# Kernel optimization log

Hardware: AMD Instinct MI355X
Metric: run time of the kernel (lower is better)

The kernel has to match this reference:

```python
import jax, jax.numpy as jnp
import numpy as np

N, V, E = 65536, 2048, 1024
TEMPERATURE = 0.5
EPS = 1e-10
LOG_PARAM_Q = -2.995732273553991


def _l2_normalize(x, axis):
    # matches torch F.normalize(p=2): x / max(||x||, 1e-12)
    n = jnp.sqrt(jnp.sum(x * x, axis=axis, keepdims=True))
    return x / jnp.maximum(n, 1e-12)


def setup_inputs() -> dict:
    key = jax.random.key(0)
    k1, k2, k3 = jax.random.split(key, 3)
    z = jax.random.normal(k1, (N, E), dtype=jnp.float32)
    emb_weight = jax.random.normal(k2, (V, E), dtype=jnp.float32)
    U = jax.random.uniform(k3, (N, V), dtype=jnp.float32)
    return {"z": z, "emb_weight": emb_weight, "U": U}


def reference(z, emb_weight, U):
    kappa_q = jnp.exp(jnp.float32(LOG_PARAM_Q)) + jnp.float32(1.0)
    zn = _l2_normalize(z, axis=1)              # [N, E]
    emb = _l2_normalize(emb_weight, axis=1)    # [V, E]
    # logit = -distances = kappa_q * z @ emb.T
    logit = kappa_q * jnp.matmul(zn, emb.T)    # [N, V]
    # gumbel-softmax sample (training branch)
    g = -jnp.log(-jnp.log(U + EPS) + EPS)
    tokens = jax.nn.softmax((logit + g) / TEMPERATURE, axis=-1)  # [N, V]
    z_q = jnp.matmul(tokens, emb)              # [N, E]
    return (tokens, z_q)
```

## Files before the change

### kernel.cpp

```cpp
#include <hip/hip_runtime.h>
#include <hip/hip_bf16.h>
#include <stdint.h>

typedef short bf16x8 __attribute__((ext_vector_type(8)));
typedef float floatx4 __attribute__((ext_vector_type(4)));

#define N_ROWS 65536
#define V_DIM 2048
#define E_DIM 1024

__device__ __forceinline__ short f2bf(float x) {
  union { float f; uint32_t u; } c; c.f = x;
  uint32_t r = (c.u + 0x7FFFu + ((c.u >> 16) & 1u)) >> 16;
  return (short)(uint16_t)r;
}
__device__ __forceinline__ float bf16f(short b) {
  union { uint32_t u; float f; } c; c.u = ((uint32_t)(uint16_t)b) << 16;
  return c.f;
}

__device__ __forceinline__ float wave_sum(float v) {
#pragma unroll
  for (int o = 32; o > 0; o >>= 1) v += __shfl_xor(v, o);
  return v;
}
__device__ __forceinline__ float wave_max(float v) {
#pragma unroll
  for (int o = 32; o > 0; o >>= 1) v = fmaxf(v, __shfl_xor(v, o));
  return v;
}

__device__ __forceinline__ void gll16(const short* g, short* l) {
  __builtin_amdgcn_global_load_lds(
      (const __attribute__((address_space(1))) void*)g,
      (__attribute__((address_space(3))) void*)l, 16, 0, 0);
}

__global__ __launch_bounds__(256) void k_norm_emb(const float* __restrict__ W,
                                                  short* __restrict__ embn,
                                                  short* __restrict__ embnT) {
  const int v = blockIdx.x;
  const int t = threadIdx.x;
  const int w = t >> 6, l = t & 63;
  const float4 val = *(const float4*)&W[(size_t)v * E_DIM + t * 4];
  float ss = val.x * val.x + val.y * val.y + val.z * val.z + val.w * val.w;
  ss = wave_sum(ss);
  __shared__ float red[4];
  if (l == 0) red[w] = ss;
  __syncthreads();
  ss = red[0] + red[1] + red[2] + red[3];
  const float inv = 1.0f / fmaxf(sqrtf(ss), 1e-12f);
  short4 o;
  o.x = f2bf(val.x * inv);
  o.y = f2bf(val.y * inv);
  o.z = f2bf(val.z * inv);
  o.w = f2bf(val.w * inv);
  *(short4*)&embn[(size_t)v * E_DIM + t * 4] = o;
  embnT[(size_t)(t * 4 + 0) * V_DIM + v] = o.x;
  embnT[(size_t)(t * 4 + 1) * V_DIM + v] = o.y;
  embnT[(size_t)(t * 4 + 2) * V_DIM + v] = o.z;
  embnT[(size_t)(t * 4 + 3) * V_DIM + v] = o.w;
}

__global__ __launch_bounds__(256) void k_norm_z(const float* __restrict__ Z,
                                                short* __restrict__ zn) {
  const int w = threadIdx.x >> 6, l = threadIdx.x & 63;
  const int row = blockIdx.x * 4 + w;
  const float* zr = Z + (size_t)row * E_DIM;
  float4 v[4];
  float ss = 0.f;
#pragma unroll
  for (int i = 0; i < 4; ++i) {
    v[i] = *(const float4*)&zr[(i * 64 + l) * 4];
    ss += v[i].x * v[i].x + v[i].y * v[i].y + v[i].z * v[i].z + v[i].w * v[i].w;
  }
  ss = wave_sum(ss);
  const float SCALE = 2.0f * (expf(-2.995732273553991f) + 1.0f);
  const float inv = SCALE / fmaxf(sqrtf(ss), 1e-12f);
  short* zo = zn + (size_t)row * E_DIM;
#pragma unroll
  for (int i = 0; i < 4; ++i) {
    short4 o;
    o.x = f2bf(v[i].x * inv);
    o.y = f2bf(v[i].y * inv);
    o.z = f2bf(v[i].z * inv);
    o.w = f2bf(v[i].w * inv);
    *(short4*)&zo[(i * 64 + l) * 4] = o;
  }
}

template <int KDIM, int NBX, int EPI>
__global__ __launch_bounds__(512, 2) void k_gemm8(
    const short* __restrict__ A, const short* __restrict__ B,
    const float* __restrict__ U, short* __restrict__ Pb,
    float* __restrict__ partials, const float* __restrict__ invsum,
    float* __restrict__ C, float* __restrict__ tokens, int cpx) {
  __shared__ __align__(16) short Sm[65536];
  const int NT = KDIM / 32;
  const int tid = threadIdx.x;
  const int wv = tid >> 6, lane = tid & 63;
  const int lr = lane & 15, lh = lane >> 4;
  const int wr = wv >> 2, wc = wv & 3;
  const int d = blockIdx.x;
  const int L = (d & 7) * cpx + (d >> 3);
  const int by = L / NBX, bx = L % NBX;
  const int m0 = by * 256, n0 = bx * 256;
  const int sg = (((lane & 3) ^ ((lane >> 2) & 3) ^ ((lane >> 4) & 3)) << 3);
  const int srow = wv * 16 + (lane >> 2);
  const short* gA = A + (size_t)(m0 + srow) * KDIM + sg;
  const short* gB = B + (size_t)(n0 + srow) * KDIM + sg;
  const int fslot = lh ^ ((lr ^ (lr >> 2)) & 3);
  const int aoff = wr * 8192 + lr * 64 + fslot * 16;
  const int boff = wc * 4096 + lr * 64 + fslot * 16;

  float inv0 = 0.f, inv1 = 0.f;
  if (EPI == 1) {
    inv0 = invsum[m0 + srow];
    inv1 = invsum[m0 + 128 + srow];
  }

#pragma unroll
  for (int t = 0; t < 2; ++t) {
#pragma unroll
    for (int q = 0; q < 2; ++q) {
      gll16(gA + (size_t)(q * 128) * KDIM + t * 32, Sm + t * 8192 + q * 4096 + wv * 512);
      gll16(gB + (size_t)(q * 128) * KDIM + t * 32, Sm + 32768 + t * 8192 + q * 4096 + wv * 512);
    }
  }
  asm volatile("s_waitcnt vmcnt(4)" ::: "memory");
  __builtin_amdgcn_s_barrier();
  __builtin_amdgcn_sched_barrier(0);

  floatx4 acc[8][4] = {};

#define DO_TILE(KT, STAGE, VMN, TOKW_)                                              \
  {                                                                                 \
    const int cb_ = (KT) & 3;                                                       \
    const char* Ab_ = (const char*)Sm + cb_ * 16384;                                \
    const char* Bb_ = (const char*)Sm + 65536 + cb_ * 16384;                        \
    short* An_ = Sm + (((KT) + 2) & 3) * 8192;                                      \
    short* Bn_ = Sm + 32768 + (((KT) + 2) & 3) * 8192;                              \
    const size_t kc_ = (size_t)((KT) + 2) * 32;                                     \
    bf16x8 bfr[4], af[4];                                                           \
     \
    _Pragma("unroll")                                                               \
    for (int n = 0; n < 4; ++n) bfr[n] = *(const bf16x8*)(Bb_ + boff + n * 1024);   \
    _Pragma("unroll")                                                               \
    for (int i = 0; i < 4; ++i) af[i] = *(const bf16x8*)(Ab_ + aoff + i * 1024);    \
    if (STAGE) {                                                                    \
      gll16(gA + kc_, An_ + wv * 512);                                              \
      gll16(gA + (size_t)128 * KDIM + kc_, An_ + 4096 + wv * 512);                  \
    }                                                                               \
    __builtin_amdgcn_s_barrier();                                                   \
    asm volatile("s_waitcnt lgkmcnt(0)" ::: "memory");                              \
    __builtin_amdgcn_sched_barrier(0);                                              \
    __builtin_amdgcn_s_setprio(1);                                                  \
    _Pragma("unroll")                                                               \
    for (int i = 0; i < 4; ++i) {                                                   \
      _Pragma("unroll")                                                             \
      for (int n = 0; n < 4; ++n)                                                   \
        acc[i][n] =                                                                 \
            __builtin_amdgcn_mfma_f32_16x16x32_bf16(af[i], bfr[n], acc[i][n], 0, 0, 0); \
    }                                                                               \
    __builtin_amdgcn_s_setprio(0);                                                  \
    __builtin_amdgcn_s_barrier();                                                   \
     \
    _Pragma("unroll")                                                               \
    for (int i = 0; i < 4; ++i)                                                     \
      af[i] = *(const bf16x8*)(Ab_ + aoff + 4096 + i * 1024);                       \
    if (STAGE) {                                                                    \
      gll16(gB + kc_, Bn_ + wv * 512);                                              \
      gll16(gB + (size_t)128 * KDIM + kc_, Bn_ + 4096 + wv * 512);                  \
    }                                                                               \
    __builtin_amdgcn_s_barrier();                                                   \
    asm volatile("s_waitcnt lgkmcnt(0)" ::: "memory");                              \
    __builtin_amdgcn_sched_barrier(0);                                              \
    __builtin_amdgcn_s_setprio(1);                                                  \
    _Pragma("unroll")                                                               \
    for (int i = 0; i < 4; ++i) {                                                   \
      _Pragma("unroll")                                                             \
      for (int n = 0; n < 4; ++n)                                                   \
        acc[4 + i][n] =                                                             \
            __builtin_amdgcn_mfma_f32_16x16x32_bf16(af[i], bfr[n], acc[4 + i][n], 0, 0, 0); \
    }                                                                               \
    __builtin_amdgcn_s_setprio(0);                                                  \
    if (TOKW_) {    \
      const short* myA_ = Sm + cb_ * 8192 + wv * 512 + lane * 8;                    \
      const bf16x8 v0_ = *(const bf16x8*)myA_;                                      \
      const bf16x8 v1_ = *(const bf16x8*)(myA_ + 4096);                             \
      const size_t c0_ = (size_t)(KT) * 32 + sg;                                    \
      float4 a_, b_;                                                                \
      a_.x = bf16f(v0_[0]) * inv0; a_.y = bf16f(v0_[1]) * inv0;                     \
      a_.z = bf16f(v0_[2]) * inv0; a_.w = bf16f(v0_[3]) * inv0;                     \
      b_.x = bf16f(v0_[4]) * inv0; b_.y = bf16f(v0_[5]) * inv0;                     \
      b_.z = bf16f(v0_[6]) * inv0; b_.w = bf16f(v0_[7]) * inv0;                     \
      *(float4*)&tokens[(size_t)(m0 + srow) * KDIM + c0_] = a_;                     \
      *(float4*)&tokens[(size_t)(m0 + srow) * KDIM + c0_ + 4] = b_;                 \
      a_.x = bf16f(v1_[0]) * inv1; a_.y = bf16f(v1_[1]) * inv1;                     \
      a_.z = bf16f(v1_[2]) * inv1; a_.w = bf16f(v1_[3]) * inv1;                     \
      b_.x = bf16f(v1_[4]) * inv1; b_.y = bf16f(v1_[5]) * inv1;                     \
      b_.z = bf16f(v1_[6]) * inv1; b_.w = bf16f(v1_[7]) * inv1;                     \
      *(float4*)&tokens[(size_t)(m0 + 128 + srow) * KDIM + c0_] = a_;               \
      *(float4*)&tokens[(size_t)(m0 + 128 + srow) * KDIM + c0_ + 4] = b_;           \
    }                                                                               \
    asm volatile("s_waitcnt vmcnt(" #VMN ")" ::: "memory");                         \
    __builtin_amdgcn_s_barrier();                                                   \
    __builtin_amdgcn_sched_barrier(0);                                              \
  }

  if (EPI == 0) {
    for (int kt = 0; kt < NT - 2; ++kt) DO_TILE(kt, 1, 4, 0);
    DO_TILE(NT - 2, 0, 0, 0);
    DO_TILE(NT - 1, 0, 0, 0);
  } else {
    const int s = bx * 16;
    int kt = 0;
    for (; kt < s; ++kt) DO_TILE(kt, 1, 4, 0);
    DO_TILE(kt, 1, 8, 1);
    ++kt;
    for (; kt < s + 16 && kt < NT - 2; ++kt) DO_TILE(kt, 1, 12, 1);
    if (kt == s + 16) {
      DO_TILE(kt, 1, 8, 0);
      ++kt;
    }
    for (; kt < NT - 2; ++kt) DO_TILE(kt, 1, 4, 0);
    DO_TILE(NT - 2, 0, 0, ((NT - 2) >> 4) == bx);
    DO_TILE(NT - 1, 0, 0, ((NT - 1) >> 4) == bx);
  }
#undef DO_TILE

  const int gr0 = m0 + wr * 128 + lh * 4;
  const int gc0 = n0 + wc * 64 + lr;
  if (EPI == 0) {
    float rs[8][4] = {};
#pragma unroll
    for (int m = 0; m < 8; ++m)
#pragma unroll
      for (int n = 0; n < 4; ++n) {
        const int col = gc0 + n * 16;
#pragma unroll
        for (int j = 0; j < 4; ++j) {
          const int row = gr0 + m * 16 + j;
          const size_t idx = (size_t)row * V_DIM + col;
          const float u = U[idx];
          const float e = __expf(acc[m][n][j] - 2.f * __logf(-__logf(u + 1e-10f) + 1e-10f));
          const short eb = f2bf(e);
          Pb[idx] = eb;
          rs[m][j] += bf16f(eb);
        }
      }
#pragma unroll
    for (int m = 0; m < 8; ++m)
#pragma unroll
      for (int j = 0; j < 4; ++j) {
        float s = rs[m][j];
        s += __shfl_xor(s, 1); s += __shfl_xor(s, 2);
        s += __shfl_xor(s, 4); s += __shfl_xor(s, 8);
        if (lr == 0)
          partials[(size_t)(gr0 + m * 16 + j) * 32 + bx * 4 + wc] = s;
      }
  } else {
#pragma unroll
    for (int m = 0; m < 8; ++m)
#pragma unroll
      for (int j = 0; j < 4; ++j) {
        const int row = gr0 + m * 16 + j;
        const float s = invsum[row];
#pragma unroll
        for (int n = 0; n < 4; ++n)
          C[(size_t)row * E_DIM + gc0 + n * 16] = acc[m][n][j] * s;
      }
  }
}

__global__ __launch_bounds__(256) void k_rowsum_inv(const float* __restrict__ partials,
                                                    float* __restrict__ invsum) {
  const int r = blockIdx.x * 256 + threadIdx.x;
  const float4* p = (const float4*)&partials[(size_t)r * 32];
  float s = 0.f;
#pragma unroll
  for (int i = 0; i < 8; ++i) { float4 v = p[i]; s += v.x + v.y + v.z + v.w; }
  invsum[r] = 1.f / s;
}

__global__ __launch_bounds__(256) void k_gemm_nt(const short* __restrict__ A,
                                                 const short* __restrict__ B,
                                                 float* __restrict__ C,
                                                 int lda, int ldb, int ldc, int K) {
  __shared__ __align__(16) short As[128][64];
  __shared__ __align__(16) short Bs[128][64];
  const int t = threadIdx.x;
  const int w = t >> 6, l = t & 63;
  const int lr = l & 15, lh = l >> 4;
  const int m0 = blockIdx.y * 128, n0 = blockIdx.x * 128;
  const int wm = (w >> 1) * 64, wn = (w & 1) * 64;
  floatx4 acc[4][4] = {};
  for (int k0 = 0; k0 < K; k0 += 64) {
    __syncthreads();
#pragma unroll
    for (int i = 0; i < 4; ++i) {
      const int c = i * 256 + t;
      const int r = c >> 3, c8 = (c & 7) * 8;
      *(bf16x8*)&As[r][c8] = *(const bf16x8*)&A[(size_t)(m0 + r) * lda + k0 + c8];
      *(bf16x8*)&Bs[r][c8] = *(const bf16x8*)&B[(size_t)(n0 + r) * ldb + k0 + c8];
    }
    __syncthreads();
#pragma unroll
    for (int kk = 0; kk < 64; kk += 32) {
      bf16x8 af[4], bfr[4];
#pragma unroll
      for (int m = 0; m < 4; ++m) af[m] = *(const bf16x8*)&As[wm + m * 16 + lr][kk + lh * 8];
#pragma unroll
      for (int n = 0; n < 4; ++n) bfr[n] = *(const bf16x8*)&Bs[wn + n * 16 + lr][kk + lh * 8];
#pragma unroll
      for (int m = 0; m < 4; ++m)
#pragma unroll
        for (int n = 0; n < 4; ++n)
          acc[m][n] = __builtin_amdgcn_mfma_f32_16x16x32_bf16(af[m], bfr[n], acc[m][n], 0, 0, 0);
    }
  }
#pragma unroll
  for (int m = 0; m < 4; ++m)
#pragma unroll
    for (int n = 0; n < 4; ++n) {
      const int col = n0 + wn + n * 16 + lr;
#pragma unroll
      for (int j = 0; j < 4; ++j)
        C[(size_t)(m0 + wm + m * 16 + lh * 4 + j) * ldc + col] = acc[m][n][j];
    }
}

__global__ __launch_bounds__(256) void k_gemm_nt_f32a(const float* __restrict__ A,
                                                      const short* __restrict__ B,
                                                      float* __restrict__ C,
                                                      int lda, int ldb, int ldc, int K) {
  __shared__ __align__(16) short As[128][64];
  __shared__ __align__(16) short Bs[128][64];
  const int t = threadIdx.x;
  const int w = t >> 6, l = t & 63;
  const int lr = l & 15, lh = l >> 4;
  const int m0 = blockIdx.y * 128, n0 = blockIdx.x * 128;
  const int wm = (w >> 1) * 64, wn = (w & 1) * 64;
  floatx4 acc[4][4] = {};
  for (int k0 = 0; k0 < K; k0 += 64) {
    __syncthreads();
#pragma unroll
    for (int i = 0; i < 4; ++i) {
      const int c = i * 256 + t;
      const int r = c >> 3, c8 = (c & 7) * 8;
      const float4 a0 = *(const float4*)&A[(size_t)(m0 + r) * lda + k0 + c8];
      const float4 a1 = *(const float4*)&A[(size_t)(m0 + r) * lda + k0 + c8 + 4];
      bf16x8 va;
      va[0] = f2bf(a0.x); va[1] = f2bf(a0.y); va[2] = f2bf(a0.z); va[3] = f2bf(a0.w);
      va[4] = f2bf(a1.x); va[5] = f2bf(a1.y); va[6] = f2bf(a1.z); va[7] = f2bf(a1.w);
      *(bf16x8*)&As[r][c8] = va;
      *(bf16x8*)&Bs[r][c8] = *(const bf16x8*)&B[(size_t)(n0 + r) * ldb + k0 + c8];
    }
    __syncthreads();
#pragma unroll
    for (int kk = 0; kk < 64; kk += 32) {
      bf16x8 af[4], bfr[4];
#pragma unroll
      for (int m = 0; m < 4; ++m) af[m] = *(const bf16x8*)&As[wm + m * 16 + lr][kk + lh * 8];
#pragma unroll
      for (int n = 0; n < 4; ++n) bfr[n] = *(const bf16x8*)&Bs[wn + n * 16 + lr][kk + lh * 8];
#pragma unroll
      for (int m = 0; m < 4; ++m)
#pragma unroll
        for (int n = 0; n < 4; ++n)
          acc[m][n] = __builtin_amdgcn_mfma_f32_16x16x32_bf16(af[m], bfr[n], acc[m][n], 0, 0, 0);
    }
  }
#pragma unroll
  for (int m = 0; m < 4; ++m)
#pragma unroll
    for (int n = 0; n < 4; ++n) {
      const int col = n0 + wn + n * 16 + lr;
#pragma unroll
      for (int j = 0; j < 4; ++j)
        C[(size_t)(m0 + wm + m * 16 + lh * 4 + j) * ldc + col] = acc[m][n][j];
    }
}

__global__ __launch_bounds__(256) void k_gumbel_softmax(float* __restrict__ S,
                                                        const float* __restrict__ U) {
  const int t = threadIdx.x;
  const int w = t >> 6, l = t & 63;
  const size_t base = (size_t)blockIdx.x * V_DIM + t * 8;
  const float4 s0 = *(const float4*)&S[base];
  const float4 s1 = *(const float4*)&S[base + 4];
  const float4 u0 = *(const float4*)&U[base];
  const float4 u1 = *(const float4*)&U[base + 4];
  float x[8];
  x[0] = s0.x - 2.f * __logf(-__logf(u0.x + 1e-10f) + 1e-10f);
  x[1] = s0.y - 2.f * __logf(-__logf(u0.y + 1e-10f) + 1e-10f);
  x[2] = s0.z - 2.f * __logf(-__logf(u0.z + 1e-10f) + 1e-10f);
  x[3] = s0.w - 2.f * __logf(-__logf(u0.w + 1e-10f) + 1e-10f);
  x[4] = s1.x - 2.f * __logf(-__logf(u1.x + 1e-10f) + 1e-10f);
  x[5] = s1.y - 2.f * __logf(-__logf(u1.y + 1e-10f) + 1e-10f);
  x[6] = s1.z - 2.f * __logf(-__logf(u1.z + 1e-10f) + 1e-10f);
  x[7] = s1.w - 2.f * __logf(-__logf(u1.w + 1e-10f) + 1e-10f);
  float lm = x[0];
#pragma unroll
  for (int i = 1; i < 8; ++i) lm = fmaxf(lm, x[i]);
  lm = wave_max(lm);
  __shared__ float redA[4], redB[4];
  if (l == 0) redA[w] = lm;
  __syncthreads();
  const float m = fmaxf(fmaxf(redA[0], redA[1]), fmaxf(redA[2], redA[3]));
  float p[8];
  float ls = 0.f;
#pragma unroll
  for (int i = 0; i < 8; ++i) { p[i] = __expf(x[i] - m); ls += p[i]; }
  ls = wave_sum(ls);
  if (l == 0) redB[w] = ls;
  __syncthreads();
  const float inv = 1.0f / (redB[0] + redB[1] + redB[2] + redB[3]);
  float4 o0 = make_float4(p[0] * inv, p[1] * inv, p[2] * inv, p[3] * inv);
  float4 o1 = make_float4(p[4] * inv, p[5] * inv, p[6] * inv, p[7] * inv);
  *(float4*)&S[base] = o0;
  *(float4*)&S[base + 4] = o1;
}

extern "C" void kernel_launch(void* const* d_in, const int* in_sizes, int n_in,
                              void* d_out, int out_size, void* d_ws, size_t ws_size,
                              hipStream_t stream) {
  const float* z = (const float*)d_in[0];
  const float* W = (const float*)d_in[1];
  const float* U = (const float*)d_in[2];
  float* tokens = (float*)d_out;
  float* zq = tokens + (size_t)N_ROWS * V_DIM;
  short* zn = (short*)zq;

  short* embn = (short*)d_ws;
  short* embnT = embn + (size_t)V_DIM * E_DIM;

  const size_t NEED = (size_t)V_DIM * E_DIM * 2 * 2
                    + (size_t)N_ROWS * 32 * 4
                    + (size_t)N_ROWS * 4
                    + (size_t)N_ROWS * V_DIM * 2;

  k_norm_emb<<<V_DIM, 256, 0, stream>>>(W, embn, embnT);
  k_norm_z<<<N_ROWS / 4, 256, 0, stream>>>(z, zn);

  if (ws_size >= NEED) {
    float* partials = (float*)(embnT + (size_t)V_DIM * E_DIM);
    float* invsum = partials + (size_t)N_ROWS * 32;
    short* Pb = (short*)(invsum + N_ROWS);
    k_gemm8<E_DIM, 8, 0><<<2048, 512, 0, stream>>>(
        zn, embn, U, Pb, partials, nullptr, nullptr, nullptr, 2048 / 8);
    k_rowsum_inv<<<N_ROWS / 256, 256, 0, stream>>>(partials, invsum);
    k_gemm8<V_DIM, 4, 1><<<1024, 512, 0, stream>>>(
        Pb, embnT, nullptr, nullptr, nullptr, invsum, zq, tokens, 1024 / 8);
  } else {
    k_gemm_nt<<<dim3(V_DIM / 128, N_ROWS / 128), 256, 0, stream>>>(
        zn, embn, tokens, E_DIM, E_DIM, V_DIM, E_DIM);
    k_gumbel_softmax<<<N_ROWS, 256, 0, stream>>>(tokens, U);
    k_gemm_nt_f32a<<<dim3(E_DIM / 128, N_ROWS / 128), 256, 0, stream>>>(
        tokens, embnT, zq, V_DIM, V_DIM, E_DIM, V_DIM);
  }
}
```

Measured before the change: 926.0 us.

## Compute logit GEMM in FP8 e4m3 with a dedicated FP8 MFMA kernel

The normalization kernels now also emit FP8 e4m3 copies of the normalized z and embedding rows. A new FP8 GEMM kernel consumes them with the fp8 MFMA instruction, using half-size LDS tiles and a higher occupancy bound, and keeps the fused Gumbel-softmax exp epilogue. The goal is to halve operand bandwidth and use the faster FP8 matrix path for the first GEMM. In exchange, logits lose precision before a temperature-scaled exponent, which risks accuracy tolerance failures, and the normalization kernels do extra conversion work and writes.

```diff
diff --git a/kernel.cpp b/kernel.cpp
--- a/kernel.cpp
+++ b/kernel.cpp
@@ -18,6 +18,21 @@
   union { uint32_t u; float f; } c; c.u = ((uint32_t)(uint16_t)b) << 16;
   return c.f;
 }
+__device__ __forceinline__ uint32_t f2e4m3(float x) {
+  union { float f; uint32_t u; } c; c.f = x;
+  const uint32_t s = (c.u >> 24) & 0x80u;
+  float ax = fabsf(x);
+  uint32_t code;
+  if (ax < 0.015625f) {
+    code = (uint32_t)__float2int_rn(ax * 512.0f);
+  } else {
+    c.f = ax;
+    uint32_t r = c.u + 0x7FFFFu + ((c.u >> 20) & 1u);
+    code = (r >> 20) - (120u << 3);
+    if (code > 0x7Eu) code = 0x7Eu;
+  }
+  return s | code;
+}
 
 __device__ __forceinline__ float wave_sum(float v) {
 #pragma unroll
@@ -30,7 +45,7 @@
   return v;
 }
 
-__device__ __forceinline__ void gll16(const short* g, short* l) {
+__device__ __forceinline__ void gll16(const void* g, void* l) {
   __builtin_amdgcn_global_load_lds(
       (const __attribute__((address_space(1))) void*)g,
       (__attribute__((address_space(3))) void*)l, 16, 0, 0);
@@ -38,7 +53,8 @@
 
 __global__ __launch_bounds__(256) void k_norm_emb(const float* __restrict__ W,
                                                   short* __restrict__ embn,
-                                                  short* __restrict__ embnT) {
+                                                  short* __restrict__ embnT,
+                                                  unsigned char* __restrict__ embn8) {
   const int v = blockIdx.x;
   const int t = threadIdx.x;
   const int w = t >> 6, l = t & 63;
@@ -60,10 +76,14 @@
   embnT[(size_t)(t * 4 + 1) * V_DIM + v] = o.y;
   embnT[(size_t)(t * 4 + 2) * V_DIM + v] = o.z;
   embnT[(size_t)(t * 4 + 3) * V_DIM + v] = o.w;
+  const uint32_t p = f2e4m3(val.x * inv) | (f2e4m3(val.y * inv) << 8) |
+                     (f2e4m3(val.z * inv) << 16) | (f2e4m3(val.w * inv) << 24);
+  *(uint32_t*)&embn8[(size_t)v * E_DIM + t * 4] = p;
 }
 
 __global__ __launch_bounds__(256) void k_norm_z(const float* __restrict__ Z,
-                                                short* __restrict__ zn) {
+                                                short* __restrict__ zn,
+                                                unsigned char* __restrict__ zn8) {
   const int w = threadIdx.x >> 6, l = threadIdx.x & 63;
   const int row = blockIdx.x * 4 + w;
   const float* zr = Z + (size_t)row * E_DIM;
@@ -78,6 +98,7 @@
   const float SCALE = 2.0f * (expf(-2.995732273553991f) + 1.0f);
   const float inv = SCALE / fmaxf(sqrtf(ss), 1e-12f);
   short* zo = zn + (size_t)row * E_DIM;
+  unsigned char* zo8 = zn8 + (size_t)row * E_DIM;
 #pragma unroll
   for (int i = 0; i < 4; ++i) {
     short4 o;
@@ -86,15 +107,135 @@
     o.z = f2bf(v[i].z * inv);
     o.w = f2bf(v[i].w * inv);
     *(short4*)&zo[(i * 64 + l) * 4] = o;
-  }
-}
-
-template <int KDIM, int NBX, int EPI>
+    const uint32_t p = f2e4m3(v[i].x * inv) | (f2e4m3(v[i].y * inv) << 8) |
+                       (f2e4m3(v[i].z * inv) << 16) | (f2e4m3(v[i].w * inv) << 24);
+    *(uint32_t*)&zo8[(i * 64 + l) * 4] = p;
+  }
+}
+
+__global__ __launch_bounds__(512, 4) void k_gemm_f8(
+    const unsigned char* __restrict__ A8, const unsigned char* __restrict__ B8,
+    const float* __restrict__ U, short* __restrict__ Pb,
+    float* __restrict__ partials, int cpx) {
+  __shared__ __align__(16) char Sm[65536];
+  const int NT = E_DIM / 32;
+  const int tid = threadIdx.x;
+  const int wv = tid >> 6, lane = tid & 63;
+  const int lr = lane & 15, lh = lane >> 4;
+  const int wr = wv >> 2, wc = wv & 3;
+  const int d = blockIdx.x;
+  const int L = (d & 7) * cpx + (d >> 3);
+  const int by = L >> 3, bx = L & 7;
+  const int m0 = by * 256, n0 = bx * 256;
+  const int sg8 = (((lane & 1) ^ ((lane >> 3) & 1)) << 4);
+  const int R8 = tid >> 1;
+  const unsigned char* gA = A8 + (size_t)(m0 + R8) * E_DIM + sg8;
+  const unsigned char* gB = B8 + (size_t)(n0 + R8) * E_DIM + sg8;
+  const int g_ = (lh ^ (((lr >> 2) & 1) << 1)) * 8;
+  const int aoff = wr * 4096 + lr * 32 + g_;
+  const int boff = wc * 2048 + lr * 32 + g_;
+
+#pragma unroll
+  for (int t = 0; t < 2; ++t) {
+    gll16(gA + t * 32, Sm + t * 8192 + wv * 1024);
+    gll16(gB + t * 32, Sm + 32768 + t * 8192 + wv * 1024);
+  }
+  asm volatile("s_waitcnt vmcnt(2)" ::: "memory");
+  __builtin_amdgcn_s_barrier();
+  __builtin_amdgcn_sched_barrier(0);
+
+  floatx4 acc[8][4] = {};
+
+#define DO_TILE(KT, STAGE, VMN)                                                     \
+  {                                                                                 \
+    const int cb_ = (KT) & 3;                                                       \
+    const char* Ab_ = Sm + cb_ * 8192;                                              \
+    const char* Bb_ = Sm + 32768 + cb_ * 8192;                                      \
+    char* An_ = Sm + (((KT) + 2) & 3) * 8192;                                       \
+    char* Bn_ = Sm + 32768 + (((KT) + 2) & 3) * 8192;                               \
+    const size_t kc_ = (size_t)((KT) + 2) * 32;                                     \
+    long bfr[4], af[4];                                                             \
+                  \
+    _Pragma("unroll")                                                               \
+    for (int n = 0; n < 4; ++n) bfr[n] = *(const long*)(Bb_ + boff + n * 512);      \
+    _Pragma("unroll")                                                               \
+    for (int i = 0; i < 4; ++i) af[i] = *(const long*)(Ab_ + aoff + i * 512);       \
+    if (STAGE) gll16(gA + kc_, An_ + wv * 1024);                                    \
+    __builtin_amdgcn_s_barrier();                                                   \
+    asm volatile("s_waitcnt lgkmcnt(0)" ::: "memory");                              \
+    __builtin_amdgcn_sched_barrier(0);                                              \
+    __builtin_amdgcn_s_setprio(1);                                                  \
+    _Pragma("unroll")                                                               \
+    for (int i = 0; i < 4; ++i) {                                                   \
+      _Pragma("unroll")                                                             \
+      for (int n = 0; n < 4; ++n)                                                   \
+        acc[i][n] =                                                                 \
+            __builtin_amdgcn_mfma_f32_16x16x32_fp8_fp8(af[i], bfr[n], acc[i][n], 0, 0, 0); \
+    }                                                                               \
+    __builtin_amdgcn_s_setprio(0);                                                  \
+    __builtin_amdgcn_s_barrier();                                                   \
+                             \
+    _Pragma("unroll")                                                               \
+    for (int i = 0; i < 4; ++i) af[i] = *(const long*)(Ab_ + aoff + 2048 + i * 512);\
+    if (STAGE) gll16(gB + kc_, Bn_ + wv * 1024);                                    \
+    __builtin_amdgcn_s_barrier();                                                   \
+    asm volatile("s_waitcnt lgkmcnt(0)" ::: "memory");                              \
+    __builtin_amdgcn_sched_barrier(0);                                              \
+    __builtin_amdgcn_s_setprio(1);                                                  \
+    _Pragma("unroll")                                                               \
+    for (int i = 0; i < 4; ++i) {                                                   \
+      _Pragma("unroll")                                                             \
+      for (int n = 0; n < 4; ++n)                                                   \
+        acc[4 + i][n] =                                                             \
+            __builtin_amdgcn_mfma_f32_16x16x32_fp8_fp8(af[i], bfr[n], acc[4 + i][n], 0, 0, 0); \
+    }                                                                               \
+    __builtin_amdgcn_s_setprio(0);                                                  \
+    asm volatile("s_waitcnt vmcnt(" #VMN ")" ::: "memory");                         \
+    __builtin_amdgcn_s_barrier();                                                   \
+    __builtin_amdgcn_sched_barrier(0);                                              \
+  }
+
+  for (int kt = 0; kt < NT - 2; ++kt) DO_TILE(kt, 1, 2);
+  DO_TILE(NT - 2, 0, 0);
+  DO_TILE(NT - 1, 0, 0);
+#undef DO_TILE
+
+  const int gr0 = m0 + wr * 128 + lh * 4;
+  const int gc0 = n0 + wc * 64 + lr;
+  float rs[8][4] = {};
+#pragma unroll
+  for (int m = 0; m < 8; ++m)
+#pragma unroll
+    for (int n = 0; n < 4; ++n) {
+      const int col = gc0 + n * 16;
+#pragma unroll
+      for (int j = 0; j < 4; ++j) {
+        const int row = gr0 + m * 16 + j;
+        const size_t idx = (size_t)row * V_DIM + col;
+        const float u = U[idx];
+        const float e = __expf(acc[m][n][j] - 2.f * __logf(-__logf(u + 1e-10f) + 1e-10f));
+        const short eb = f2bf(e);
+        Pb[idx] = eb;
+        rs[m][j] += bf16f(eb);
+      }
+    }
+#pragma unroll
+  for (int m = 0; m < 8; ++m)
+#pragma unroll
+    for (int j = 0; j < 4; ++j) {
+      float s = rs[m][j];
+      s += __shfl_xor(s, 1); s += __shfl_xor(s, 2);
+      s += __shfl_xor(s, 4); s += __shfl_xor(s, 8);
+      if (lr == 0)
+        partials[(size_t)(gr0 + m * 16 + j) * 32 + bx * 4 + wc] = s;
+    }
+}
+
+template <int KDIM, int NBX>
 __global__ __launch_bounds__(512, 2) void k_gemm8(
     const short* __restrict__ A, const short* __restrict__ B,
-    const float* __restrict__ U, short* __restrict__ Pb,
-    float* __restrict__ partials, const float* __restrict__ invsum,
-    float* __restrict__ C, float* __restrict__ tokens, int cpx) {
+    const float* __restrict__ invsum, float* __restrict__ C,
+    float* __restrict__ tokens, int cpx) {
   __shared__ __align__(16) short Sm[65536];
   const int NT = KDIM / 32;
   const int tid = threadIdx.x;
@@ -113,11 +254,8 @@
   const int aoff = wr * 8192 + lr * 64 + fslot * 16;
   const int boff = wc * 4096 + lr * 64 + fslot * 16;
 
-  float inv0 = 0.f, inv1 = 0.f;
-  if (EPI == 1) {
-    inv0 = invsum[m0 + srow];
-    inv1 = invsum[m0 + 128 + srow];
-  }
+  float inv0 = invsum[m0 + srow];
+  float inv1 = invsum[m0 + 128 + srow];
 
 #pragma unroll
   for (int t = 0; t < 2; ++t) {
@@ -142,7 +280,6 @@
     short* Bn_ = Sm + 32768 + (((KT) + 2) & 3) * 8192;                              \
     const size_t kc_ = (size_t)((KT) + 2) * 32;                                     \
     bf16x8 bfr[4], af[4];                                                           \
-     \
     _Pragma("unroll")                                                               \
     for (int n = 0; n < 4; ++n) bfr[n] = *(const bf16x8*)(Bb_ + boff + n * 1024);   \
     _Pragma("unroll")                                                               \
@@ -164,7 +301,6 @@
     }                                                                               \
     __builtin_amdgcn_s_setprio(0);                                                  \
     __builtin_amdgcn_s_barrier();                                                   \
-     \
     _Pragma("unroll")                                                               \
     for (int i = 0; i < 4; ++i)                                                     \
       af[i] = *(const bf16x8*)(Ab_ + aoff + 4096 + i * 1024);                       \
@@ -184,7 +320,7 @@
             __builtin_amdgcn_mfma_f32_16x16x32_bf16(af[i], bfr[n], acc[4 + i][n], 0, 0, 0); \
     }                                                                               \
     __builtin_amdgcn_s_setprio(0);                                                  \
-    if (TOKW_) {    \
+    if (TOKW_) {                                                                    \
       const short* myA_ = Sm + cb_ * 8192 + wv * 512 + lane * 8;                    \
       const bf16x8 v0_ = *(const bf16x8*)myA_;                                      \
       const bf16x8 v1_ = *(const bf16x8*)(myA_ + 4096);                             \
@@ -208,11 +344,7 @@
     __builtin_amdgcn_sched_barrier(0);                                              \
   }
 
-  if (EPI == 0) {
-    for (int kt = 0; kt < NT - 2; ++kt) DO_TILE(kt, 1, 4, 0);
-    DO_TILE(NT - 2, 0, 0, 0);
-    DO_TILE(NT - 1, 0, 0, 0);
-  } else {
+  {
     const int s = bx * 16;
     int kt = 0;
     for (; kt < s; ++kt) DO_TILE(kt, 1, 4, 0);
@@ -231,46 +363,16 @@
 
   const int gr0 = m0 + wr * 128 + lh * 4;
   const int gc0 = n0 + wc * 64 + lr;
-  if (EPI == 0) {
-    float rs[8][4] = {};
-#pragma unroll
-    for (int m = 0; m < 8; ++m)
-#pragma unroll
-      for (int n = 0; n < 4; ++n) {
-        const int col = gc0 + n * 16;
-#pragma unroll
-        for (int j = 0; j < 4; ++j) {
-          const int row = gr0 + m * 16 + j;
-          const size_t idx = (size_t)row * V_DIM + col;
-          const float u = U[idx];
-          const float e = __expf(acc[m][n][j] - 2.f * __logf(-__logf(u + 1e-10f) + 1e-10f));
-          const short eb = f2bf(e);
-          Pb[idx] = eb;
-          rs[m][j] += bf16f(eb);
-        }
-      }
-#pragma unroll
-    for (int m = 0; m < 8; ++m)
-#pragma unroll
-      for (int j = 0; j < 4; ++j) {
-        float s = rs[m][j];
-        s += __shfl_xor(s, 1); s += __shfl_xor(s, 2);
-        s += __shfl_xor(s, 4); s += __shfl_xor(s, 8);
-        if (lr == 0)
-          partials[(size_t)(gr0 + m * 16 + j) * 32 + bx * 4 + wc] = s;
-      }
-  } else {
-#pragma unroll
-    for (int m = 0; m < 8; ++m)
-#pragma unroll
-      for (int j = 0; j < 4; ++j) {
-        const int row = gr0 + m * 16 + j;
-        const float s = invsum[row];
-#pragma unroll
-        for (int n = 0; n < 4; ++n)
-          C[(size_t)row * E_DIM + gc0 + n * 16] = acc[m][n][j] * s;
-      }
-  }
+#pragma unroll
+  for (int m = 0; m < 8; ++m)
+#pragma unroll
+    for (int j = 0; j < 4; ++j) {
+      const int row = gr0 + m * 16 + j;
+      const float s = invsum[row];
+#pragma unroll
+      for (int n = 0; n < 4; ++n)
+        C[(size_t)row * E_DIM + gc0 + n * 16] = acc[m][n][j] * s;
+    }
 }
 
 __global__ __launch_bounds__(256) void k_rowsum_inv(const float* __restrict__ partials,
@@ -431,27 +533,30 @@
   float* tokens = (float*)d_out;
   float* zq = tokens + (size_t)N_ROWS * V_DIM;
   short* zn = (short*)zq;
+  unsigned char* zn8 =
+      (unsigned char*)zq + (size_t)N_ROWS * E_DIM * 2;
 
   short* embn = (short*)d_ws;
   short* embnT = embn + (size_t)V_DIM * E_DIM;
+  unsigned char* embn8 = (unsigned char*)(embnT + (size_t)V_DIM * E_DIM);
 
   const size_t NEED = (size_t)V_DIM * E_DIM * 2 * 2
+                    + (size_t)V_DIM * E_DIM
                     + (size_t)N_ROWS * 32 * 4
                     + (size_t)N_ROWS * 4
                     + (size_t)N_ROWS * V_DIM * 2;
 
-  k_norm_emb<<<V_DIM, 256, 0, stream>>>(W, embn, embnT);
-  k_norm_z<<<N_ROWS / 4, 256, 0, stream>>>(z, zn);
+  k_norm_emb<<<V_DIM, 256, 0, stream>>>(W, embn, embnT, embn8);
+  k_norm_z<<<N_ROWS / 4, 256, 0, stream>>>(z, zn, zn8);
 
   if (ws_size >= NEED) {
-    float* partials = (float*)(embnT + (size_t)V_DIM * E_DIM);
+    float* partials = (float*)(embn8 + (size_t)V_DIM * E_DIM);
     float* invsum = partials + (size_t)N_ROWS * 32;
     short* Pb = (short*)(invsum + N_ROWS);
-    k_gemm8<E_DIM, 8, 0><<<2048, 512, 0, stream>>>(
-        zn, embn, U, Pb, partials, nullptr, nullptr, nullptr, 2048 / 8);
+    k_gemm_f8<<<2048, 512, 0, stream>>>(zn8, embn8, U, Pb, partials, 2048 / 8);
     k_rowsum_inv<<<N_ROWS / 256, 256, 0, stream>>>(partials, invsum);
-    k_gemm8<V_DIM, 4, 1><<<1024, 512, 0, stream>>>(
-        Pb, embnT, nullptr, nullptr, nullptr, invsum, zq, tokens, 1024 / 8);
+    k_gemm8<V_DIM, 4><<<1024, 512, 0, stream>>>(
+        Pb, embnT, invsum, zq, tokens, 1024 / 8);
   } else {
     k_gemm_nt<<<dim3(V_DIM / 128, N_ROWS / 128), 256, 0, stream>>>(
         zn, embn, tokens, E_DIM, E_DIM, V_DIM, E_DIM);
```

Measured after the change: 2.949 ms. 3.18x slower.
